# Kernel optimization log

Hardware: AMD Instinct MI355X
Metric: run time of the kernel (lower is better)

The kernel has to match this reference:

```python
import jax, jax.numpy as jnp
import numpy as np

D_MODEL = 384
HEAD_SIZE = 64
B, T = 64, 512


def setup_inputs() -> dict:
    key = jax.random.key(0)
    kx, kq, kk, kv = jax.random.split(key, 4)
    x = jax.random.normal(kx, (B, T, D_MODEL), dtype=jnp.float32)
    Wq = jax.random.normal(kq, (D_MODEL, HEAD_SIZE), dtype=jnp.float32) * 0.02
    Wk = jax.random.normal(kk, (D_MODEL, HEAD_SIZE), dtype=jnp.float32) * 0.02
    Wv = jax.random.normal(kv, (D_MODEL, HEAD_SIZE), dtype=jnp.float32) * 0.02
    return {"x": x, "Wq": Wq, "Wk": Wk, "Wv": Wv}


def reference(x, Wq, Wk, Wv):
    # x: [B, T, C]; projections (bias-free linear layers)
    q = jnp.einsum("btc,ch->bth", x, Wq)  # [B, T, H]
    k = jnp.einsum("btc,ch->bth", x, Wk)
    v = jnp.einsum("btc,ch->bth", x, Wv)
    Tn = x.shape[1]
    scale = 1.0 / jnp.sqrt(jnp.float32(k.shape[-1]))
    wei = jnp.einsum("bqh,bkh->bqk", q, k) * scale  # [B, T, T]
    causal = jnp.tril(jnp.ones((Tn, Tn), dtype=bool))
    wei = jnp.where(causal, wei, -jnp.inf)
    wei = jax.nn.softmax(wei, axis=-1)
    # dropout omitted (eval mode) for deterministic reference
    out = jnp.einsum("bqk,bkh->bqh", wei, v)  # [B, T, H]
    return out
```

## Files before the change

kernel.cpp:

```cpp
#include <hip/hip_runtime.h>
#include <math.h>

#define NB 64
#define NT 512
#define NC 384
#define NH 64

typedef __attribute__((ext_vector_type(8))) short bf16x8;
typedef __attribute__((ext_vector_type(4))) float f32x4;

__device__ __forceinline__ unsigned short f2bf(float f) {
  unsigned int u = __float_as_uint(f);
  return (unsigned short)((u + 0x7FFFu + ((u >> 16) & 1u)) >> 16);
}
__device__ __forceinline__ unsigned int pk2bf(float a, float b) {
  return (unsigned int)f2bf(a) | ((unsigned int)f2bf(b) << 16);
}

__global__ __launch_bounds__(256) void wtrans_kernel(
    const float* __restrict__ Wq, const float* __restrict__ Wk,
    const float* __restrict__ Wv, unsigned short* __restrict__ Wt) {
  int id = blockIdx.x * 256 + threadIdx.x;
  if (id >= 3 * NC * NH) return;
  int m = id / (NC * NH);
  int r = id % (NC * NH);
  int c = r / NH;
  int h = r % NH;
  const float* W = (m == 0) ? Wq : ((m == 1) ? Wk : Wv);
  Wt[(m * NH + h) * NC + c] = f2bf(W[c * NH + h]);
}

#define XS 392
__global__ __launch_bounds__(384, 3) void proj_kernel(
    const float* __restrict__ x, const unsigned short* __restrict__ Wt,
    unsigned short* __restrict__ q, unsigned short* __restrict__ k,
    unsigned short* __restrict__ vt) {
  __shared__ unsigned short xs[64 * XS];
  const int t = threadIdx.x;
  const int m0 = blockIdx.x * 64;
  const int w = t / 64, l = t & 63, mi = l & 15, quad = l >> 4;

#pragma unroll 4
  for (int i = 0; i < 16; ++i) {
    int u = t + i * 384;
    int row = u / 96;
    int cp = (u % 96) * 4;
    float4 a = *(const float4*)(x + (size_t)(m0 + row) * NC + cp);
    ushort4 bb;
    bb.x = f2bf(a.x); bb.y = f2bf(a.y); bb.z = f2bf(a.z); bb.w = f2bf(a.w);
    *(ushort4*)&xs[row * XS + cp] = bb;
  }

  bf16x8 bfr[2][12];
#pragma unroll
  for (int ntl = 0; ntl < 2; ++ntl) {
    const unsigned short* wr =
        Wt + (size_t)((w * 2 + ntl) * 16 + mi) * NC + quad * 8;
#pragma unroll
    for (int kc = 0; kc < 12; ++kc)
      bfr[ntl][kc] = *(const bf16x8*)(wr + kc * 32);
  }
  __syncthreads();

  f32x4 acc[2][4];
  const f32x4 zero = {0.f, 0.f, 0.f, 0.f};
#pragma unroll
  for (int i = 0; i < 2; ++i)
#pragma unroll
    for (int j = 0; j < 4; ++j) acc[i][j] = zero;

#pragma unroll
  for (int msub = 0; msub < 4; ++msub) {
#pragma unroll
    for (int kc = 0; kc < 12; ++kc) {
      bf16x8 a = *(const bf16x8*)&xs[(msub * 16 + mi) * XS + kc * 32 + quad * 8];
      acc[0][msub] =
          __builtin_amdgcn_mfma_f32_16x16x32_bf16(a, bfr[0][kc], acc[0][msub], 0, 0, 0);
      acc[1][msub] =
          __builtin_amdgcn_mfma_f32_16x16x32_bf16(a, bfr[1][kc], acc[1][msub], 0, 0, 0);
    }
  }

  if (w < 4) {
    unsigned short* dst = (w < 2) ? q : k;
    const float sc = (w < 2) ? 0.125f : 1.0f;
#pragma unroll
    for (int ntl = 0; ntl < 2; ++ntl) {
      int tile = w * 2 + ntl;
      int h = (tile & 3) * 16 + mi;
#pragma unroll
      for (int msub = 0; msub < 4; ++msub)
#pragma unroll
        for (int r = 0; r < 4; ++r)
          dst[(size_t)(m0 + msub * 16 + quad * 4 + r) * NH + h] =
              f2bf(acc[ntl][msub][r] * sc);
    }
  } else {
    int bb = m0 >> 9, t0 = m0 & 511;
#pragma unroll
    for (int ntl = 0; ntl < 2; ++ntl) {
      int tile = w * 2 + ntl;
      int h = (tile & 3) * 16 + mi;
#pragma unroll
      for (int msub = 0; msub < 4; ++msub) {
        ushort4 s;
        s.x = f2bf(acc[ntl][msub][0]);
        s.y = f2bf(acc[ntl][msub][1]);
        s.z = f2bf(acc[ntl][msub][2]);
        s.w = f2bf(acc[ntl][msub][3]);
        *(ushort4*)&vt[((size_t)bb * NH + h) * NT + t0 + msub * 16 + quad * 4] = s;
      }
    }
  }
}

#define PSTR 72
__global__ __launch_bounds__(64) void attn_kernel(
    const unsigned short* __restrict__ q, const unsigned short* __restrict__ k,
    const unsigned short* __restrict__ vt, float* __restrict__ out) {
  __shared__ unsigned short ps[16 * PSTR];
  const int l = threadIdx.x;
  const int mi = l & 15, quad = l >> 4;
  const int bx = blockIdx.x;
  const int qi = 31 - (bx >> 6);
  const int b = bx & 63;

  const unsigned short* qrow = q + ((size_t)b * NT + qi * 16 + mi) * NH;
  bf16x8 qb0 = *(const bf16x8*)(qrow + quad * 8);
  bf16x8 qb1 = *(const bf16x8*)(qrow + 32 + quad * 8);

  f32x4 accO[4];
  const f32x4 zero = {0.f, 0.f, 0.f, 0.f};
#pragma unroll
  for (int i = 0; i < 4; ++i) accO[i] = zero;
  float mrow = -INFINITY, lrow = 0.f;

  const int ktmax = (qi * 16 + 15) >> 6;
  for (int kt = 0; kt <= ktmax; ++kt) {
    const unsigned short* kb = k + ((size_t)b * NT + kt * 64) * NH;
    const unsigned short* vb = vt + (size_t)b * NH * NT + kt * 64;
    bf16x8 ka0[4], ka1[4], va0[4], va1[4];
#pragma unroll
    for (int nt = 0; nt < 4; ++nt) {
      const unsigned short* kr = kb + (size_t)(nt * 16 + mi) * NH + quad * 8;
      ka0[nt] = *(const bf16x8*)kr;
      ka1[nt] = *(const bf16x8*)(kr + 32);
      const unsigned short* vr = vb + (size_t)(nt * 16 + mi) * NT + quad * 8;
      va0[nt] = *(const bf16x8*)vr;
      va1[nt] = *(const bf16x8*)(vr + 32);
    }

    float p[4][4];
#pragma unroll
    for (int nt = 0; nt < 4; ++nt) {
      f32x4 z = zero;
      z = __builtin_amdgcn_mfma_f32_16x16x32_bf16(ka0[nt], qb0, z, 0, 0, 0);
      z = __builtin_amdgcn_mfma_f32_16x16x32_bf16(ka1[nt], qb1, z, 0, 0, 0);
#pragma unroll
      for (int r = 0; r < 4; ++r) p[nt][r] = z[r];
    }

    if (kt == ktmax) {
#pragma unroll
      for (int nt = 0; nt < 4; ++nt)
#pragma unroll
        for (int r = 0; r < 4; ++r)
          if (kt * 64 + nt * 16 + quad * 4 + r > qi * 16 + mi)
            p[nt][r] = -INFINITY;
    }

    float vmax = -INFINITY;
#pragma unroll
    for (int nt = 0; nt < 4; ++nt)
#pragma unroll
      for (int r = 0; r < 4; ++r) vmax = fmaxf(vmax, p[nt][r]);
    vmax = fmaxf(vmax, __shfl_xor(vmax, 16));
    vmax = fmaxf(vmax, __shfl_xor(vmax, 32));
    float mn = fmaxf(mrow, vmax);
    float alpha = __expf(mrow - mn);
    mrow = mn;

    float rsum = 0.f;
#pragma unroll
    for (int nt = 0; nt < 4; ++nt)
#pragma unroll
      for (int r = 0; r < 4; ++r) {
        p[nt][r] = __expf(p[nt][r] - mn);
        rsum += p[nt][r];
      }
    rsum += __shfl_xor(rsum, 16);
    rsum += __shfl_xor(rsum, 32);
    lrow = lrow * alpha + rsum;

#pragma unroll
    for (int nt = 0; nt < 4; ++nt) {
      uint2 pk;
      pk.x = pk2bf(p[nt][0], p[nt][1]);
      pk.y = pk2bf(p[nt][2], p[nt][3]);
      *(uint2*)&ps[mi * PSTR + nt * 16 + quad * 4] = pk;
    }
    bf16x8 pa0 = *(const bf16x8*)&ps[mi * PSTR + quad * 8];
    bf16x8 pa1 = *(const bf16x8*)&ps[mi * PSTR + 32 + quad * 8];

    float av[4];
#pragma unroll
    for (int r = 0; r < 4; ++r) av[r] = __shfl(alpha, quad * 4 + r);
#pragma unroll
    for (int hi = 0; hi < 4; ++hi)
#pragma unroll
      for (int r = 0; r < 4; ++r) accO[hi][r] *= av[r];

#pragma unroll
    for (int hi = 0; hi < 4; ++hi) {
      accO[hi] = __builtin_amdgcn_mfma_f32_16x16x32_bf16(pa0, va0[hi], accO[hi], 0, 0, 0);
      accO[hi] = __builtin_amdgcn_mfma_f32_16x16x32_bf16(pa1, va1[hi], accO[hi], 0, 0, 0);
    }
  }

  float inv = 1.f / lrow;
  const size_t obase = ((size_t)b * NT + qi * 16) * NH;
#pragma unroll
  for (int r = 0; r < 4; ++r) {
    float iv = __shfl(inv, quad * 4 + r);
#pragma unroll
    for (int hi = 0; hi < 4; ++hi)
      out[obase + (size_t)(quad * 4 + r) * NH + hi * 16 + mi] = accO[hi][r] * iv;
  }
}

extern "C" void kernel_launch(void* const* d_in, const int* in_sizes, int n_in,
                              void* d_out, int out_size, void* d_ws, size_t ws_size,
                              hipStream_t stream) {
  const float* x  = (const float*)d_in[0];
  const float* Wq = (const float*)d_in[1];
  const float* Wk = (const float*)d_in[2];
  const float* Wv = (const float*)d_in[3];

  unsigned short* Wt = (unsigned short*)d_ws;
  unsigned short* qb = Wt + 192 * 384;
  unsigned short* kb = qb + 32768 * 64;
  unsigned short* vtb = kb + 32768 * 64;
  float* out = (float*)d_out;

  wtrans_kernel<<<288, 256, 0, stream>>>(Wq, Wk, Wv, Wt);
  proj_kernel<<<512, 384, 0, stream>>>(x, Wt, qb, kb, vtb);
  attn_kernel<<<2048, 64, 0, stream>>>(qb, kb, vtb, out);
}
```

Measured before the change: 121.9 us.

## Split attention KV loop across two waves per block and merge partials

The attention kernel now runs two waves per block. Each wave handles alternating 64-key tiles with its own online-softmax state and its own P staging buffer. Wave 1 writes its partial output, max and sum to shared memory, and wave 0 rescales and combines them before the final normalization. The aim is to shorten the serial per-wave KV loop and put more waves on each CU, at the cost of extra LDS, a block barrier and a merge step.

```diff
diff --git a/kernel.cpp b/kernel.cpp
--- a/kernel.cpp
+++ b/kernel.cpp
@@ -115,11 +115,16 @@
 }
 
 #define PSTR 72
-__global__ __launch_bounds__(64) void attn_kernel(
+__global__ __launch_bounds__(128) void attn_kernel(
     const unsigned short* __restrict__ q, const unsigned short* __restrict__ k,
     const unsigned short* __restrict__ vt, float* __restrict__ out) {
-  __shared__ unsigned short ps[16 * PSTR];
-  const int l = threadIdx.x;
+  __shared__ unsigned short ps[2][16 * PSTR];
+  __shared__ float obuf[16 * 64];
+  __shared__ float mlbuf[2][16];
+
+  const int t = threadIdx.x;
+  const int w = t >> 6;
+  const int l = t & 63;
   const int mi = l & 15, quad = l >> 4;
   const int bx = blockIdx.x;
   const int qi = 31 - (bx >> 6);
@@ -136,7 +141,7 @@
   float mrow = -INFINITY, lrow = 0.f;
 
   const int ktmax = (qi * 16 + 15) >> 6;
-  for (int kt = 0; kt <= ktmax; ++kt) {
+  for (int kt = w; kt <= ktmax; kt += 2) {
     const unsigned short* kb = k + ((size_t)b * NT + kt * 64) * NH;
     const unsigned short* vb = vt + (size_t)b * NH * NT + kt * 64;
     bf16x8 ka0[4], ka1[4], va0[4], va1[4];
@@ -197,10 +202,10 @@
       uint2 pk;
       pk.x = pk2bf(p[nt][0], p[nt][1]);
       pk.y = pk2bf(p[nt][2], p[nt][3]);
-      *(uint2*)&ps[mi * PSTR + nt * 16 + quad * 4] = pk;
-    }
-    bf16x8 pa0 = *(const bf16x8*)&ps[mi * PSTR + quad * 8];
-    bf16x8 pa1 = *(const bf16x8*)&ps[mi * PSTR + 32 + quad * 8];
+      *(uint2*)&ps[w][mi * PSTR + nt * 16 + quad * 4] = pk;
+    }
+    bf16x8 pa0 = *(const bf16x8*)&ps[w][mi * PSTR + quad * 8];
+    bf16x8 pa1 = *(const bf16x8*)&ps[w][mi * PSTR + 32 + quad * 8];
 
     float av[4];
 #pragma unroll
@@ -217,14 +222,39 @@
     }
   }
 
-  float inv = 1.f / lrow;
-  const size_t obase = ((size_t)b * NT + qi * 16) * NH;
-#pragma unroll
-  for (int r = 0; r < 4; ++r) {
-    float iv = __shfl(inv, quad * 4 + r);
+  if (w == 1) {
 #pragma unroll
     for (int hi = 0; hi < 4; ++hi)
-      out[obase + (size_t)(quad * 4 + r) * NH + hi * 16 + mi] = accO[hi][r] * iv;
+#pragma unroll
+      for (int r = 0; r < 4; ++r)
+        obuf[(quad * 4 + r) * 64 + hi * 16 + mi] = accO[hi][r];
+    if (quad == 0) {
+      mlbuf[0][mi] = mrow;
+      mlbuf[1][mi] = lrow;
+    }
+  }
+  __syncthreads();
+  if (w == 0) {
+    float m1 = mlbuf[0][mi], l1 = mlbuf[1][mi];
+    float mf = fmaxf(mrow, m1);
+    float a0 = __expf(mrow - mf);
+    float a1 = __expf(m1 - mf);
+    float lf = a0 * lrow + a1 * l1;
+    float inv = 1.f / lf;
+
+    const size_t obase = ((size_t)b * NT + qi * 16) * NH;
+#pragma unroll
+    for (int r = 0; r < 4; ++r) {
+      float a0r = __shfl(a0, quad * 4 + r);
+      float a1r = __shfl(a1, quad * 4 + r);
+      float ivr = __shfl(inv, quad * 4 + r);
+#pragma unroll
+      for (int hi = 0; hi < 4; ++hi) {
+        float o1 = obuf[(quad * 4 + r) * 64 + hi * 16 + mi];
+        out[obase + (size_t)(quad * 4 + r) * NH + hi * 16 + mi] =
+            (a0r * accO[hi][r] + a1r * o1) * ivr;
+      }
+    }
   }
 }
 
@@ -244,5 +274,5 @@
 
   wtrans_kernel<<<288, 256, 0, stream>>>(Wq, Wk, Wv, Wt);
   proj_kernel<<<512, 384, 0, stream>>>(x, Wt, qb, kb, vtb);
-  attn_kernel<<<2048, 64, 0, stream>>>(qb, kb, vtb, out);
-}
+  attn_kernel<<<2048, 128, 0, stream>>>(qb, kb, vtb, out);
+}
```

New measurement: 123.0 us. Within noise of the previous version (+0.9%).

## Fuse weight transpose, projection and attention into one persistent kernel with grid barriers

Applied to the files above, without the earlier changes.

Replaces the three separate launches with a single persistent kernel of 256 blocks that performs the weight transpose, the QKV projection (two 64-row tiles per block) and the attention, separated by atomic-counter grid barriers. A memset resets the counters on each call. The aim is to remove launch and inter-kernel gaps. In exchange, attention now runs only 1536 concurrent waves in two passes rather than 2048 independent blocks, which loses load balancing for the causal work. The barrier also relies on all 256 blocks being co-resident.

```diff
diff --git a/kernel.cpp b/kernel.cpp
--- a/kernel.cpp
+++ b/kernel.cpp
@@ -17,214 +17,242 @@
   return (unsigned int)f2bf(a) | ((unsigned int)f2bf(b) << 16);
 }
 
-__global__ __launch_bounds__(256) void wtrans_kernel(
-    const float* __restrict__ Wq, const float* __restrict__ Wk,
-    const float* __restrict__ Wv, unsigned short* __restrict__ Wt) {
-  int id = blockIdx.x * 256 + threadIdx.x;
-  if (id >= 3 * NC * NH) return;
-  int m = id / (NC * NH);
-  int r = id % (NC * NH);
-  int c = r / NH;
-  int h = r % NH;
-  const float* W = (m == 0) ? Wq : ((m == 1) ? Wk : Wv);
-  Wt[(m * NH + h) * NC + c] = f2bf(W[c * NH + h]);
+__device__ __forceinline__ void grid_barrier(unsigned* cnt) {
+  __syncthreads();
+  if (threadIdx.x == 0) {
+    __threadfence();
+    atomicAdd(cnt, 1u);
+    while (atomicAdd(cnt, 0u) < 256u) __builtin_amdgcn_s_sleep(8);
+  }
+  __syncthreads();
+  __threadfence();
 }
 
 #define XS 392
-__global__ __launch_bounds__(384, 3) void proj_kernel(
-    const float* __restrict__ x, const unsigned short* __restrict__ Wt,
+#define PSTR 72
+
+__global__ __launch_bounds__(384, 2) void fused_kernel(
+    const float* __restrict__ x, const float* __restrict__ Wq,
+    const float* __restrict__ Wk, const float* __restrict__ Wv,
+    unsigned* __restrict__ cnt, unsigned short* __restrict__ Wt,
     unsigned short* __restrict__ q, unsigned short* __restrict__ k,
-    unsigned short* __restrict__ vt) {
+    unsigned short* __restrict__ vt, float* __restrict__ out) {
   __shared__ unsigned short xs[64 * XS];
+  const int bx = blockIdx.x;
   const int t = threadIdx.x;
-  const int m0 = blockIdx.x * 64;
   const int w = t / 64, l = t & 63, mi = l & 15, quad = l >> 4;
 
+  {
+    int id = bx * 384 + t;
+    if (id < 3 * NC * NH) {
+      int m = id / (NC * NH);
+      int r = id % (NC * NH);
+      int c = r / NH;
+      int h = r % NH;
+      const float* W = (m == 0) ? Wq : ((m == 1) ? Wk : Wv);
+      Wt[(m * NH + h) * NC + c] = f2bf(W[c * NH + h]);
+    }
+  }
+  grid_barrier(cnt);
+
+  {
+    bf16x8 bfr[2][12];
+#pragma unroll
+    for (int ntl = 0; ntl < 2; ++ntl) {
+      const unsigned short* wr =
+          Wt + (size_t)((w * 2 + ntl) * 16 + mi) * NC + quad * 8;
+#pragma unroll
+      for (int kc = 0; kc < 12; ++kc)
+        bfr[ntl][kc] = *(const bf16x8*)(wr + kc * 32);
+    }
+
+    for (int half = 0; half < 2; ++half) {
+      const int m0 = bx * 128 + half * 64;
+      if (half) __syncthreads();
+
 #pragma unroll 4
-  for (int i = 0; i < 16; ++i) {
-    int u = t + i * 384;
-    int row = u / 96;
-    int cp = (u % 96) * 4;
-    float4 a = *(const float4*)(x + (size_t)(m0 + row) * NC + cp);
-    ushort4 bb;
-    bb.x = f2bf(a.x); bb.y = f2bf(a.y); bb.z = f2bf(a.z); bb.w = f2bf(a.w);
-    *(ushort4*)&xs[row * XS + cp] = bb;
-  }
-
-  bf16x8 bfr[2][12];
-#pragma unroll
-  for (int ntl = 0; ntl < 2; ++ntl) {
-    const unsigned short* wr =
-        Wt + (size_t)((w * 2 + ntl) * 16 + mi) * NC + quad * 8;
-#pragma unroll
-    for (int kc = 0; kc < 12; ++kc)
-      bfr[ntl][kc] = *(const bf16x8*)(wr + kc * 32);
-  }
-  __syncthreads();
-
-  f32x4 acc[2][4];
-  const f32x4 zero = {0.f, 0.f, 0.f, 0.f};
-#pragma unroll
-  for (int i = 0; i < 2; ++i)
-#pragma unroll
-    for (int j = 0; j < 4; ++j) acc[i][j] = zero;
-
-#pragma unroll
-  for (int msub = 0; msub < 4; ++msub) {
-#pragma unroll
-    for (int kc = 0; kc < 12; ++kc) {
-      bf16x8 a = *(const bf16x8*)&xs[(msub * 16 + mi) * XS + kc * 32 + quad * 8];
-      acc[0][msub] =
-          __builtin_amdgcn_mfma_f32_16x16x32_bf16(a, bfr[0][kc], acc[0][msub], 0, 0, 0);
-      acc[1][msub] =
-          __builtin_amdgcn_mfma_f32_16x16x32_bf16(a, bfr[1][kc], acc[1][msub], 0, 0, 0);
-    }
-  }
-
-  if (w < 4) {
-    unsigned short* dst = (w < 2) ? q : k;
-    const float sc = (w < 2) ? 0.125f : 1.0f;
-#pragma unroll
-    for (int ntl = 0; ntl < 2; ++ntl) {
-      int tile = w * 2 + ntl;
-      int h = (tile & 3) * 16 + mi;
-#pragma unroll
-      for (int msub = 0; msub < 4; ++msub)
-#pragma unroll
-        for (int r = 0; r < 4; ++r)
-          dst[(size_t)(m0 + msub * 16 + quad * 4 + r) * NH + h] =
-              f2bf(acc[ntl][msub][r] * sc);
-    }
-  } else {
-    int bb = m0 >> 9, t0 = m0 & 511;
-#pragma unroll
-    for (int ntl = 0; ntl < 2; ++ntl) {
-      int tile = w * 2 + ntl;
-      int h = (tile & 3) * 16 + mi;
+      for (int i = 0; i < 16; ++i) {
+        int u = t + i * 384;
+        int row = u / 96;
+        int cp = (u % 96) * 4;
+        float4 a = *(const float4*)(x + (size_t)(m0 + row) * NC + cp);
+        ushort4 bb;
+        bb.x = f2bf(a.x); bb.y = f2bf(a.y); bb.z = f2bf(a.z); bb.w = f2bf(a.w);
+        *(ushort4*)&xs[row * XS + cp] = bb;
+      }
+      __syncthreads();
+
+      f32x4 acc[2][4];
+      const f32x4 zero = {0.f, 0.f, 0.f, 0.f};
+#pragma unroll
+      for (int i = 0; i < 2; ++i)
+#pragma unroll
+        for (int j = 0; j < 4; ++j) acc[i][j] = zero;
+
 #pragma unroll
       for (int msub = 0; msub < 4; ++msub) {
-        ushort4 s;
-        s.x = f2bf(acc[ntl][msub][0]);
-        s.y = f2bf(acc[ntl][msub][1]);
-        s.z = f2bf(acc[ntl][msub][2]);
-        s.w = f2bf(acc[ntl][msub][3]);
-        *(ushort4*)&vt[((size_t)bb * NH + h) * NT + t0 + msub * 16 + quad * 4] = s;
-      }
-    }
-  }
-}
-
-#define PSTR 72
-__global__ __launch_bounds__(64) void attn_kernel(
-    const unsigned short* __restrict__ q, const unsigned short* __restrict__ k,
-    const unsigned short* __restrict__ vt, float* __restrict__ out) {
-  __shared__ unsigned short ps[16 * PSTR];
-  const int l = threadIdx.x;
-  const int mi = l & 15, quad = l >> 4;
-  const int bx = blockIdx.x;
-  const int qi = 31 - (bx >> 6);
-  const int b = bx & 63;
-
-  const unsigned short* qrow = q + ((size_t)b * NT + qi * 16 + mi) * NH;
-  bf16x8 qb0 = *(const bf16x8*)(qrow + quad * 8);
-  bf16x8 qb1 = *(const bf16x8*)(qrow + 32 + quad * 8);
-
-  f32x4 accO[4];
-  const f32x4 zero = {0.f, 0.f, 0.f, 0.f};
-#pragma unroll
-  for (int i = 0; i < 4; ++i) accO[i] = zero;
-  float mrow = -INFINITY, lrow = 0.f;
-
-  const int ktmax = (qi * 16 + 15) >> 6;
-  for (int kt = 0; kt <= ktmax; ++kt) {
-    const unsigned short* kb = k + ((size_t)b * NT + kt * 64) * NH;
-    const unsigned short* vb = vt + (size_t)b * NH * NT + kt * 64;
-    bf16x8 ka0[4], ka1[4], va0[4], va1[4];
-#pragma unroll
-    for (int nt = 0; nt < 4; ++nt) {
-      const unsigned short* kr = kb + (size_t)(nt * 16 + mi) * NH + quad * 8;
-      ka0[nt] = *(const bf16x8*)kr;
-      ka1[nt] = *(const bf16x8*)(kr + 32);
-      const unsigned short* vr = vb + (size_t)(nt * 16 + mi) * NT + quad * 8;
-      va0[nt] = *(const bf16x8*)vr;
-      va1[nt] = *(const bf16x8*)(vr + 32);
-    }
-
-    float p[4][4];
-#pragma unroll
-    for (int nt = 0; nt < 4; ++nt) {
-      f32x4 z = zero;
-      z = __builtin_amdgcn_mfma_f32_16x16x32_bf16(ka0[nt], qb0, z, 0, 0, 0);
-      z = __builtin_amdgcn_mfma_f32_16x16x32_bf16(ka1[nt], qb1, z, 0, 0, 0);
-#pragma unroll
-      for (int r = 0; r < 4; ++r) p[nt][r] = z[r];
-    }
-
-    if (kt == ktmax) {
-#pragma unroll
-      for (int nt = 0; nt < 4; ++nt)
-#pragma unroll
-        for (int r = 0; r < 4; ++r)
-          if (kt * 64 + nt * 16 + quad * 4 + r > qi * 16 + mi)
-            p[nt][r] = -INFINITY;
-    }
-
-    float vmax = -INFINITY;
-#pragma unroll
-    for (int nt = 0; nt < 4; ++nt)
-#pragma unroll
-      for (int r = 0; r < 4; ++r) vmax = fmaxf(vmax, p[nt][r]);
-    vmax = fmaxf(vmax, __shfl_xor(vmax, 16));
-    vmax = fmaxf(vmax, __shfl_xor(vmax, 32));
-    float mn = fmaxf(mrow, vmax);
-    float alpha = __expf(mrow - mn);
-    mrow = mn;
-
-    float rsum = 0.f;
-#pragma unroll
-    for (int nt = 0; nt < 4; ++nt)
+#pragma unroll
+        for (int kc = 0; kc < 12; ++kc) {
+          bf16x8 a =
+              *(const bf16x8*)&xs[(msub * 16 + mi) * XS + kc * 32 + quad * 8];
+          acc[0][msub] = __builtin_amdgcn_mfma_f32_16x16x32_bf16(
+              a, bfr[0][kc], acc[0][msub], 0, 0, 0);
+          acc[1][msub] = __builtin_amdgcn_mfma_f32_16x16x32_bf16(
+              a, bfr[1][kc], acc[1][msub], 0, 0, 0);
+        }
+      }
+
+      if (w < 4) {
+        unsigned short* dst = (w < 2) ? q : k;
+        const float sc = (w < 2) ? 0.125f : 1.0f;
+#pragma unroll
+        for (int ntl = 0; ntl < 2; ++ntl) {
+          int tile = w * 2 + ntl;
+          int h = (tile & 3) * 16 + mi;
+#pragma unroll
+          for (int msub = 0; msub < 4; ++msub)
+#pragma unroll
+            for (int r = 0; r < 4; ++r)
+              dst[(size_t)(m0 + msub * 16 + quad * 4 + r) * NH + h] =
+                  f2bf(acc[ntl][msub][r] * sc);
+        }
+      } else {
+        int bb = m0 >> 9, t0 = m0 & 511;
+#pragma unroll
+        for (int ntl = 0; ntl < 2; ++ntl) {
+          int tile = w * 2 + ntl;
+          int h = (tile & 3) * 16 + mi;
+#pragma unroll
+          for (int msub = 0; msub < 4; ++msub) {
+            ushort4 s;
+            s.x = f2bf(acc[ntl][msub][0]);
+            s.y = f2bf(acc[ntl][msub][1]);
+            s.z = f2bf(acc[ntl][msub][2]);
+            s.w = f2bf(acc[ntl][msub][3]);
+            *(ushort4*)&vt[((size_t)bb * NH + h) * NT + t0 + msub * 16 +
+                           quad * 4] = s;
+          }
+        }
+      }
+    }
+  }
+  grid_barrier(cnt + 1);
+
+  {
+    unsigned short* ps = &xs[w * 16 * PSTR];
+    const int gw = bx * 6 + w;
+    const f32x4 zero = {0.f, 0.f, 0.f, 0.f};
+
+    for (int pass = 0; pass < 2; ++pass) {
+      const int ti = gw + pass * 1536;
+      if (ti >= 2048) break;
+      const int qi = 31 - (ti >> 6);
+      const int b = ti & 63;
+
+      const unsigned short* qrow = q + ((size_t)b * NT + qi * 16 + mi) * NH;
+      bf16x8 qb0 = *(const bf16x8*)(qrow + quad * 8);
+      bf16x8 qb1 = *(const bf16x8*)(qrow + 32 + quad * 8);
+
+      f32x4 accO[4];
+#pragma unroll
+      for (int i = 0; i < 4; ++i) accO[i] = zero;
+      float mrow = -INFINITY, lrow = 0.f;
+
+      const int ktmax = (qi * 16 + 15) >> 6;
+      for (int kt = 0; kt <= ktmax; ++kt) {
+        const unsigned short* kb = k + ((size_t)b * NT + kt * 64) * NH;
+        const unsigned short* vb = vt + (size_t)b * NH * NT + kt * 64;
+        bf16x8 ka0[4], ka1[4], va0[4], va1[4];
+#pragma unroll
+        for (int nt = 0; nt < 4; ++nt) {
+          const unsigned short* kr = kb + (size_t)(nt * 16 + mi) * NH + quad * 8;
+          ka0[nt] = *(const bf16x8*)kr;
+          ka1[nt] = *(const bf16x8*)(kr + 32);
+          const unsigned short* vr = vb + (size_t)(nt * 16 + mi) * NT + quad * 8;
+          va0[nt] = *(const bf16x8*)vr;
+          va1[nt] = *(const bf16x8*)(vr + 32);
+        }
+
+        float p[4][4];
+#pragma unroll
+        for (int nt = 0; nt < 4; ++nt) {
+          f32x4 z = zero;
+          z = __builtin_amdgcn_mfma_f32_16x16x32_bf16(ka0[nt], qb0, z, 0, 0, 0);
+          z = __builtin_amdgcn_mfma_f32_16x16x32_bf16(ka1[nt], qb1, z, 0, 0, 0);
+#pragma unroll
+          for (int r = 0; r < 4; ++r) p[nt][r] = z[r];
+        }
+
+        if (kt == ktmax) {
+#pragma unroll
+          for (int nt = 0; nt < 4; ++nt)
+#pragma unroll
+            for (int r = 0; r < 4; ++r)
+              if (kt * 64 + nt * 16 + quad * 4 + r > qi * 16 + mi)
+                p[nt][r] = -INFINITY;
+        }
+
+        float vmax = -INFINITY;
+#pragma unroll
+        for (int nt = 0; nt < 4; ++nt)
+#pragma unroll
+          for (int r = 0; r < 4; ++r) vmax = fmaxf(vmax, p[nt][r]);
+        vmax = fmaxf(vmax, __shfl_xor(vmax, 16));
+        vmax = fmaxf(vmax, __shfl_xor(vmax, 32));
+        float mn = fmaxf(mrow, vmax);
+        float alpha = __expf(mrow - mn);
+        mrow = mn;
+
+        float rsum = 0.f;
+#pragma unroll
+        for (int nt = 0; nt < 4; ++nt)
+#pragma unroll
+          for (int r = 0; r < 4; ++r) {
+            p[nt][r] = __expf(p[nt][r] - mn);
+            rsum += p[nt][r];
+          }
+        rsum += __shfl_xor(rsum, 16);
+        rsum += __shfl_xor(rsum, 32);
+        lrow = lrow * alpha + rsum;
+
+#pragma unroll
+        for (int nt = 0; nt < 4; ++nt) {
+          uint2 pk;
+          pk.x = pk2bf(p[nt][0], p[nt][1]);
+          pk.y = pk2bf(p[nt][2], p[nt][3]);
+          *(uint2*)&ps[mi * PSTR + nt * 16 + quad * 4] = pk;
+        }
+        bf16x8 pa0 = *(const bf16x8*)&ps[mi * PSTR + quad * 8];
+        bf16x8 pa1 = *(const bf16x8*)&ps[mi * PSTR + 32 + quad * 8];
+
+        float av[4];
+#pragma unroll
+        for (int r = 0; r < 4; ++r) av[r] = __shfl(alpha, quad * 4 + r);
+#pragma unroll
+        for (int hi = 0; hi < 4; ++hi)
+#pragma unroll
+          for (int r = 0; r < 4; ++r) accO[hi][r] *= av[r];
+
+#pragma unroll
+        for (int hi = 0; hi < 4; ++hi) {
+          accO[hi] = __builtin_amdgcn_mfma_f32_16x16x32_bf16(pa0, va0[hi],
+                                                             accO[hi], 0, 0, 0);
+          accO[hi] = __builtin_amdgcn_mfma_f32_16x16x32_bf16(pa1, va1[hi],
+                                                             accO[hi], 0, 0, 0);
+        }
+      }
+
+      float inv = 1.f / lrow;
+      const size_t obase = ((size_t)b * NT + qi * 16) * NH;
 #pragma unroll
       for (int r = 0; r < 4; ++r) {
-        p[nt][r] = __expf(p[nt][r] - mn);
-        rsum += p[nt][r];
-      }
-    rsum += __shfl_xor(rsum, 16);
-    rsum += __shfl_xor(rsum, 32);
-    lrow = lrow * alpha + rsum;
-
-#pragma unroll
-    for (int nt = 0; nt < 4; ++nt) {
-      uint2 pk;
-      pk.x = pk2bf(p[nt][0], p[nt][1]);
-      pk.y = pk2bf(p[nt][2], p[nt][3]);
-      *(uint2*)&ps[mi * PSTR + nt * 16 + quad * 4] = pk;
-    }
-    bf16x8 pa0 = *(const bf16x8*)&ps[mi * PSTR + quad * 8];
-    bf16x8 pa1 = *(const bf16x8*)&ps[mi * PSTR + 32 + quad * 8];
-
-    float av[4];
-#pragma unroll
-    for (int r = 0; r < 4; ++r) av[r] = __shfl(alpha, quad * 4 + r);
-#pragma unroll
-    for (int hi = 0; hi < 4; ++hi)
-#pragma unroll
-      for (int r = 0; r < 4; ++r) accO[hi][r] *= av[r];
-
-#pragma unroll
-    for (int hi = 0; hi < 4; ++hi) {
-      accO[hi] = __builtin_amdgcn_mfma_f32_16x16x32_bf16(pa0, va0[hi], accO[hi], 0, 0, 0);
-      accO[hi] = __builtin_amdgcn_mfma_f32_16x16x32_bf16(pa1, va1[hi], accO[hi], 0, 0, 0);
-    }
-  }
-
-  float inv = 1.f / lrow;
-  const size_t obase = ((size_t)b * NT + qi * 16) * NH;
-#pragma unroll
-  for (int r = 0; r < 4; ++r) {
-    float iv = __shfl(inv, quad * 4 + r);
-#pragma unroll
-    for (int hi = 0; hi < 4; ++hi)
-      out[obase + (size_t)(quad * 4 + r) * NH + hi * 16 + mi] = accO[hi][r] * iv;
+        float iv = __shfl(inv, quad * 4 + r);
+#pragma unroll
+        for (int hi = 0; hi < 4; ++hi)
+          out[obase + (size_t)(quad * 4 + r) * NH + hi * 16 + mi] =
+              accO[hi][r] * iv;
+      }
+    }
   }
 }
 
@@ -236,13 +264,13 @@
   const float* Wk = (const float*)d_in[2];
   const float* Wv = (const float*)d_in[3];
 
-  unsigned short* Wt = (unsigned short*)d_ws;
+  unsigned* cnt = (unsigned*)d_ws;
+  unsigned short* Wt = (unsigned short*)d_ws + 128;
   unsigned short* qb = Wt + 192 * 384;
   unsigned short* kb = qb + 32768 * 64;
   unsigned short* vtb = kb + 32768 * 64;
   float* out = (float*)d_out;
 
-  wtrans_kernel<<<288, 256, 0, stream>>>(Wq, Wk, Wv, Wt);
-  proj_kernel<<<512, 384, 0, stream>>>(x, Wt, qb, kb, vtb);
-  attn_kernel<<<2048, 64, 0, stream>>>(qb, kb, vtb, out);
-}
+  hipMemsetAsync(cnt, 0, 8, stream);
+  fused_kernel<<<256, 384, 0, stream>>>(x, Wq, Wk, Wv, cnt, Wt, qb, kb, vtb, out);
+}
```

Result: slower. 215.5 us (+76.8%).
